# Kernel optimization log

Measured on AMD Instinct MI355X. Metric: run time of the kernel, lower is better.

The kernel has to match this reference:

```python
import jax, jax.numpy as jnp
import numpy as np

EPS = 1e-5
SINKHORN_ITERS = 20
ALPHA_INIT = 0.01


def setup_inputs() -> dict:
    key = jax.random.key(0)
    ks = jax.random.split(key, 8)
    B, n, C = 8192, 4, 2048
    nC = n * C
    return {
        "x_expanded": jax.random.normal(ks[0], (B, n, C), dtype=jnp.float32),
        "rmsnorm_weight": jnp.ones((C,), dtype=jnp.float32),
        "phi_pre": 0.02 * jax.random.normal(ks[1], (n, nC), dtype=jnp.float32),
        "phi_post": 0.02 * jax.random.normal(ks[2], (n, nC), dtype=jnp.float32),
        "phi_res": 0.02 * jax.random.normal(ks[3], (n * n, nC), dtype=jnp.float32),
        "b_pre": jnp.zeros((n,), dtype=jnp.float32),
        "b_post": jnp.zeros((n,), dtype=jnp.float32),
        "b_res": jnp.zeros((n, n), dtype=jnp.float32),
        "alpha_pre": jnp.float32(ALPHA_INIT),
        "alpha_post": jnp.float32(ALPHA_INIT),
        "alpha_res": jnp.float32(ALPHA_INIT),
    }


def _rmsnorm(x, w, eps):
    # RMSNorm over the channel dim C of each stream
    ms = jnp.mean(x * x, axis=-1, keepdims=True)
    return x * jax.lax.rsqrt(ms + eps) * w


def _sinkhorn(logits, iters, eps):
    # logits: (B, n, n) -> doubly-stochastic matrix via Sinkhorn-Knopp
    m = jnp.exp(logits - jnp.max(logits, axis=(1, 2), keepdims=True))
    for _ in range(iters):
        m = m / (jnp.sum(m, axis=2, keepdims=True) + eps)  # row normalize
        m = m / (jnp.sum(m, axis=1, keepdims=True) + eps)  # col normalize
    return m


def reference(x_expanded, rmsnorm_weight, phi_pre, phi_post, phi_res,
              b_pre, b_post, b_res, alpha_pre, alpha_post, alpha_res):
    B, n, C = x_expanded.shape
    x_norm = _rmsnorm(x_expanded, rmsnorm_weight, EPS)   # (B, n, C)
    xf = x_norm.reshape(B, n * C)                         # (B, nC)

    # dynamic mixing coefficients from learned projections
    h_pre = alpha_pre * (xf @ phi_pre.T) + b_pre          # (B, n)
    h_post = alpha_post * (xf @ phi_post.T) + b_post      # (B, n)
    h_res_logits = (alpha_res * (xf @ phi_res.T) + b_res.reshape(-1)).reshape(B, n, n)

    h_res = _sinkhorn(h_res_logits, SINKHORN_ITERS, EPS)  # (B, n, n) doubly stochastic

    # blended mixing of the raw residual streams
    mixed = jnp.einsum('bij,bjc->bic', h_res, x_expanded)        # (B, n, C)
    agg = jnp.einsum('bn,bnc->bc', h_pre, x_expanded)            # (B, C)
    out = mixed + h_post[:, :, None] * agg[:, None, :]           # (B, n, C)
    return out
```

## Files before the change

### kernel.cpp

```cpp
#include <hip/hip_runtime.h>
#include <hip/hip_bf16.h>
#include <cstdint>

#define CH 2048
#define NCF 8192
#define NJ 24
#define RPB 4
#define EPS_F 1e-5f
#define SINK_ITERS 20

typedef float v4f __attribute__((ext_vector_type(4)));

__device__ __forceinline__ uint32_t bf16rne(float f) {
    uint32_t u = __float_as_uint(f);
    return (u + 0x7fffu + ((u >> 16) & 1u)) >> 16;
}

__device__ __forceinline__ float dot8(const uint4& x, const uint4& p, float acc) {
    asm("v_dot2_f32_bf16 %0, %1, %2, %0" : "+v"(acc) : "v"(x.x), "v"(p.x));
    asm("v_dot2_f32_bf16 %0, %1, %2, %0" : "+v"(acc) : "v"(x.y), "v"(p.y));
    asm("v_dot2_f32_bf16 %0, %1, %2, %0" : "+v"(acc) : "v"(x.z), "v"(p.z));
    asm("v_dot2_f32_bf16 %0, %1, %2, %0" : "+v"(acc) : "v"(x.w), "v"(p.w));
    return acc;
}

__global__ void __launch_bounds__(256) prep_phi_kernel(
    const float* __restrict__ w,
    const float* __restrict__ phi_pre,
    const float* __restrict__ phi_post,
    const float* __restrict__ phi_res,
    const float* __restrict__ alpha_pre,
    const float* __restrict__ alpha_post,
    const float* __restrict__ alpha_res,
    uint16_t* __restrict__ phiW)
{
    int idx = blockIdx.x * 256 + threadIdx.x;
    if (idx >= NJ * NCF) return;
    int j = idx / NCF;
    int k = idx - j * NCF;
    int c = k & (CH - 1);
    float v, a;
    if (j < 4)      { v = phi_pre[j * NCF + k];        a = alpha_pre[0]; }
    else if (j < 8) { v = phi_post[(j - 4) * NCF + k]; a = alpha_post[0]; }
    else            { v = phi_res[(j - 8) * NCF + k];  a = alpha_res[0]; }
    phiW[idx] = (uint16_t)bf16rne(v * a * w[c]);
}

__global__ void __launch_bounds__(512) mhc_main_kernel(
    const float* __restrict__ x,
    const uint16_t* __restrict__ phiW,
    const float* __restrict__ b_pre,
    const float* __restrict__ b_post,
    const float* __restrict__ b_res,
    float* __restrict__ out)
{
    const int t = threadIdx.x;
    const int lane = t & 63;
    const int wave = t >> 6;
    const long b0 = (long)blockIdx.x * RPB;

    __shared__ uint32_t xn[RPB][NCF / 2];
    __shared__ float4 red[RPB][8];
    __shared__ float H[RPB][24];
    __shared__ float MS[RPB][16];

    {
        const float4* xp = reinterpret_cast<const float4*>(x + b0 * NCF);
        #pragma unroll
        for (int r = 0; r < RPB; ++r) {
            float ss0, ss1, ss2, ss3;
            {
                float4 a0 = xp[r * 2048 + t];
                float4 a1 = xp[r * 2048 + t + 512];
                float4 a2 = xp[r * 2048 + t + 1024];
                float4 a3 = xp[r * 2048 + t + 1536];
                ss0 = a0.x*a0.x + a0.y*a0.y + a0.z*a0.z + a0.w*a0.w;
                ss1 = a1.x*a1.x + a1.y*a1.y + a1.z*a1.z + a1.w*a1.w;
                ss2 = a2.x*a2.x + a2.y*a2.y + a2.z*a2.z + a2.w*a2.w;
                ss3 = a3.x*a3.x + a3.y*a3.y + a3.z*a3.z + a3.w*a3.w;
                *reinterpret_cast<uint2*>(&xn[r][2*t]) =
                    make_uint2(bf16rne(a0.x) | (bf16rne(a0.y) << 16),
                               bf16rne(a0.z) | (bf16rne(a0.w) << 16));
                *reinterpret_cast<uint2*>(&xn[r][2*t + 1024]) =
                    make_uint2(bf16rne(a1.x) | (bf16rne(a1.y) << 16),
                               bf16rne(a1.z) | (bf16rne(a1.w) << 16));
                *reinterpret_cast<uint2*>(&xn[r][2*t + 2048]) =
                    make_uint2(bf16rne(a2.x) | (bf16rne(a2.y) << 16),
                               bf16rne(a2.z) | (bf16rne(a2.w) << 16));
                *reinterpret_cast<uint2*>(&xn[r][2*t + 3072]) =
                    make_uint2(bf16rne(a3.x) | (bf16rne(a3.y) << 16),
                               bf16rne(a3.z) | (bf16rne(a3.w) << 16));
            }
            #pragma unroll
            for (int m = 1; m < 64; m <<= 1) {
                ss0 += __shfl_xor(ss0, m, 64);
                ss1 += __shfl_xor(ss1, m, 64);
                ss2 += __shfl_xor(ss2, m, 64);
                ss3 += __shfl_xor(ss3, m, 64);
            }
            if (lane == 0) red[r][wave] = make_float4(ss0, ss1, ss2, ss3);
        }
    }
    __syncthreads();

    float scl[RPB][4];
    #pragma unroll
    for (int r = 0; r < RPB; ++r) {
        float sx = 0.f, sy = 0.f, sz = 0.f, sw = 0.f;
        #pragma unroll
        for (int w8 = 0; w8 < 8; ++w8) {
            float4 v = red[r][w8];
            sx += v.x; sy += v.y; sz += v.z; sw += v.w;
        }
        scl[r][0] = rsqrtf(sx * (1.0f / CH) + EPS_F);
        scl[r][1] = rsqrtf(sy * (1.0f / CH) + EPS_F);
        scl[r][2] = rsqrtf(sz * (1.0f / CH) + EPS_F);
        scl[r][3] = rsqrtf(sw * (1.0f / CH) + EPS_F);
    }

    float accT[3][RPB] = {};
    float accS[3][RPB] = {};
    {
        const uint16_t* pw = phiW + (size_t)(wave * 3) * NCF;
        const int kl = 8 * lane;
        const uint4* xr0 = reinterpret_cast<const uint4*>(xn[0]);
        const uint4* xr1 = reinterpret_cast<const uint4*>(xn[1]);
        const uint4* xr2 = reinterpret_cast<const uint4*>(xn[2]);
        const uint4* xr3 = reinterpret_cast<const uint4*>(xn[3]);

        uint4 pbuf[3][3];
        uint4 xbuf[2][4];

        #pragma unroll
        for (int jl = 0; jl < 3; ++jl) {
            pbuf[0][jl] = *reinterpret_cast<const uint4*>(pw + jl * NCF + kl);
            pbuf[1][jl] = *reinterpret_cast<const uint4*>(pw + jl * NCF + 512 + kl);
        }
        xbuf[0][0] = xr0[lane]; xbuf[0][1] = xr1[lane];
        xbuf[0][2] = xr2[lane]; xbuf[0][3] = xr3[lane];

        #pragma unroll
        for (int u = 0; u < 16; ++u) {
            const int cur = u % 3;
            const int nxt = (u + 2) % 3;
            const int xc = u & 1;
            const int xq = (u + 1) & 1;
            if (u + 1 < 16) {
                const int i1 = 64 * (u + 1) + lane;
                xbuf[xq][0] = xr0[i1]; xbuf[xq][1] = xr1[i1];
                xbuf[xq][2] = xr2[i1]; xbuf[xq][3] = xr3[i1];
            }
            if (u + 2 < 16) {
                const int k2 = 512 * (u + 2) + kl;
                #pragma unroll
                for (int jl = 0; jl < 3; ++jl)
                    pbuf[nxt][jl] = *reinterpret_cast<const uint4*>(pw + jl * NCF + k2);
            }
            #pragma unroll
            for (int jl = 0; jl < 3; ++jl) {
                accS[jl][0] = dot8(xbuf[xc][0], pbuf[cur][jl], accS[jl][0]);
                accS[jl][1] = dot8(xbuf[xc][1], pbuf[cur][jl], accS[jl][1]);
                accS[jl][2] = dot8(xbuf[xc][2], pbuf[cur][jl], accS[jl][2]);
                accS[jl][3] = dot8(xbuf[xc][3], pbuf[cur][jl], accS[jl][3]);
            }
            if ((u & 3) == 3) {
                const int s = u >> 2;
                #pragma unroll
                for (int jl = 0; jl < 3; ++jl) {
                    #pragma unroll
                    for (int r = 0; r < RPB; ++r) {
                        accT[jl][r] = fmaf(scl[r][s], accS[jl][r], accT[jl][r]);
                        accS[jl][r] = 0.f;
                    }
                }
            }
        }
    }
    {
        #pragma unroll
        for (int m = 1; m < 64; m <<= 1) {
            #pragma unroll
            for (int jl = 0; jl < 3; ++jl) {
                #pragma unroll
                for (int r = 0; r < RPB; ++r)
                    accT[jl][r] += __shfl_xor(accT[jl][r], m, 64);
            }
        }
        if (lane == 0) {
            #pragma unroll
            for (int jl = 0; jl < 3; ++jl) {
                int j = 3 * wave + jl;
                float bias;
                if (j < 4)      bias = b_pre[j];
                else if (j < 8) bias = b_post[j - 4];
                else            bias = b_res[j - 8];
                #pragma unroll
                for (int r = 0; r < RPB; ++r) H[r][j] = accT[jl][r] + bias;
            }
        }
    }
    __syncthreads();

    {
        const int r = lane >> 4;
        const int q = lane & 15;
        float L = H[r][8 + q];
        float mx = L;
        mx = fmaxf(mx, __shfl_xor(mx, 1, 64));
        mx = fmaxf(mx, __shfl_xor(mx, 2, 64));
        mx = fmaxf(mx, __shfl_xor(mx, 4, 64));
        mx = fmaxf(mx, __shfl_xor(mx, 8, 64));
        float m = __expf(L - mx);
        #pragma unroll
        for (int it = 0; it < SINK_ITERS; ++it) {
            float rs = m + __shfl_xor(m, 1, 64);
            rs += __shfl_xor(rs, 2, 64);
            m = m * __builtin_amdgcn_rcpf(rs + EPS_F);
            float cs = m + __shfl_xor(m, 4, 64);
            cs += __shfl_xor(cs, 8, 64);
            m = m * __builtin_amdgcn_rcpf(cs + EPS_F);
        }
        MS[r][q] = m;
    }

    #pragma unroll
    for (int r = 0; r < RPB; ++r) {
        const float4 hp = *reinterpret_cast<const float4*>(&H[r][0]);
        const float4 hq = *reinterpret_cast<const float4*>(&H[r][4]);
        float4 hrm[4];
        #pragma unroll
        for (int i = 0; i < 4; ++i)
            hrm[i] = *reinterpret_cast<const float4*>(&MS[r][4 * i]);
        float4 s[4];
        #pragma unroll
        for (int jj = 0; jj < 4; ++jj) {
            uint2 pk = *reinterpret_cast<const uint2*>(&xn[r][2 * t + 1024 * jj]);
            s[jj].x = __uint_as_float(pk.x << 16);
            s[jj].y = __uint_as_float(pk.x & 0xffff0000u);
            s[jj].z = __uint_as_float(pk.y << 16);
            s[jj].w = __uint_as_float(pk.y & 0xffff0000u);
        }
        float ax = hp.x*s[0].x + hp.y*s[1].x + hp.z*s[2].x + hp.w*s[3].x;
        float ay = hp.x*s[0].y + hp.y*s[1].y + hp.z*s[2].y + hp.w*s[3].y;
        float az = hp.x*s[0].z + hp.y*s[1].z + hp.z*s[2].z + hp.w*s[3].z;
        float aw = hp.x*s[0].w + hp.y*s[1].w + hp.z*s[2].w + hp.w*s[3].w;
        const float hqv[4] = {hq.x, hq.y, hq.z, hq.w};
        v4f* op = reinterpret_cast<v4f*>(out + (b0 + r) * NCF + 4 * t);
        #pragma unroll
        for (int i = 0; i < 4; ++i) {
            v4f o;
            o.x = hrm[i].x*s[0].x + hrm[i].y*s[1].x + hrm[i].z*s[2].x + hrm[i].w*s[3].x + hqv[i]*ax;
            o.y = hrm[i].x*s[0].y + hrm[i].y*s[1].y + hrm[i].z*s[2].y + hrm[i].w*s[3].y + hqv[i]*ay;
            o.z = hrm[i].x*s[0].z + hrm[i].y*s[1].z + hrm[i].z*s[2].z + hrm[i].w*s[3].z + hqv[i]*az;
            o.w = hrm[i].x*s[0].w + hrm[i].y*s[1].w + hrm[i].z*s[2].w + hrm[i].w*s[3].w + hqv[i]*aw;
            __builtin_nontemporal_store(o, op + i * 512);
        }
    }
}

extern "C" void kernel_launch(void* const* d_in, const int* in_sizes, int n_in,
                              void* d_out, int out_size, void* d_ws, size_t ws_size,
                              hipStream_t stream)
{
    const float* x        = (const float*)d_in[0];
    const float* w        = (const float*)d_in[1];
    const float* phi_pre  = (const float*)d_in[2];
    const float* phi_post = (const float*)d_in[3];
    const float* phi_res  = (const float*)d_in[4];
    const float* b_pre    = (const float*)d_in[5];
    const float* b_post   = (const float*)d_in[6];
    const float* b_res    = (const float*)d_in[7];
    const float* a_pre    = (const float*)d_in[8];
    const float* a_post   = (const float*)d_in[9];
    const float* a_res    = (const float*)d_in[10];
    float* out = (float*)d_out;
    uint16_t* phiW = (uint16_t*)d_ws;

    const int B = in_sizes[0] / NCF;

    prep_phi_kernel<<<(NJ * NCF + 255) / 256, 256, 0, stream>>>(
        w, phi_pre, phi_post, phi_res, a_pre, a_post, a_res, phiW);

    mhc_main_kernel<<<B / RPB, 512, 0, stream>>>(
        x, phiW, b_pre, b_post, b_res, out);
}
```

Measured before the change: 157.5 us.

## Quantize activations and projection weights to int8 and use int8 dot products

Replaces the bf16 staging of x and the folded phi weights with per-row and per-stream absmax int8 quantization. The projection GEMV now uses v_dot4_i32_i8 with integer accumulators. The output mixing reads the int8 values and folds the dequant scales into a fused mixing matrix. The change halves the LDS footprint and the packed-weight traffic, but adds an extra absmax pre-pass kernel and a second global read of x. It also noticeably lowers accuracy on the output path, which risks failing tolerance.

```diff
diff --git a/kernel.cpp b/kernel.cpp
--- a/kernel.cpp
+++ b/kernel.cpp
@@ -11,20 +11,17 @@
 
 typedef float v4f __attribute__((ext_vector_type(4)));
 
-__device__ __forceinline__ uint32_t bf16rne(float f) {
-    uint32_t u = __float_as_uint(f);
-    return (u + 0x7fffu + ((u >> 16) & 1u)) >> 16;
-}
-
-__device__ __forceinline__ float dot8(const uint4& x, const uint4& p, float acc) {
-    asm("v_dot2_f32_bf16 %0, %1, %2, %0" : "+v"(acc) : "v"(x.x), "v"(p.x));
-    asm("v_dot2_f32_bf16 %0, %1, %2, %0" : "+v"(acc) : "v"(x.y), "v"(p.y));
-    asm("v_dot2_f32_bf16 %0, %1, %2, %0" : "+v"(acc) : "v"(x.z), "v"(p.z));
-    asm("v_dot2_f32_bf16 %0, %1, %2, %0" : "+v"(acc) : "v"(x.w), "v"(p.w));
-    return acc;
-}
-
-__global__ void __launch_bounds__(256) prep_phi_kernel(
+__device__ __forceinline__ int dot4i8(uint32_t a, uint32_t b, int c) {
+#if __has_builtin(__builtin_amdgcn_sdot4)
+    return __builtin_amdgcn_sdot4((int)a, (int)b, c, false);
+#else
+    int d;
+    asm("v_dot4_i32_i8 %0, %1, %2, %3" : "=v"(d) : "v"(a), "v"(b), "v"(c));
+    return d;
+#endif
+}
+
+__global__ void __launch_bounds__(256) prep_amax_kernel(
     const float* __restrict__ w,
     const float* __restrict__ phi_pre,
     const float* __restrict__ phi_post,
@@ -32,7 +29,36 @@
     const float* __restrict__ alpha_pre,
     const float* __restrict__ alpha_post,
     const float* __restrict__ alpha_res,
-    uint16_t* __restrict__ phiW)
+    float* __restrict__ amaxphi)
+{
+    const int j = blockIdx.x;
+    const int t = threadIdx.x;
+    const float* src; float a;
+    if (j < 4)      { src = phi_pre  + (size_t)j * NCF;       a = alpha_pre[0]; }
+    else if (j < 8) { src = phi_post + (size_t)(j-4) * NCF;   a = alpha_post[0]; }
+    else            { src = phi_res  + (size_t)(j-8) * NCF;   a = alpha_res[0]; }
+    float m = 0.f;
+    for (int k = t; k < NCF; k += 256)
+        m = fmaxf(m, fabsf(src[k] * a * w[k & (CH - 1)]));
+    #pragma unroll
+    for (int s = 1; s < 64; s <<= 1) m = fmaxf(m, __shfl_xor(m, s, 64));
+    __shared__ float wm[4];
+    if ((t & 63) == 0) wm[t >> 6] = m;
+    __syncthreads();
+    if (t == 0)
+        amaxphi[j] = fmaxf(fmaxf(fmaxf(wm[0], wm[1]), fmaxf(wm[2], wm[3])), 1e-30f);
+}
+
+__global__ void __launch_bounds__(256) prep_quant_kernel(
+    const float* __restrict__ w,
+    const float* __restrict__ phi_pre,
+    const float* __restrict__ phi_post,
+    const float* __restrict__ phi_res,
+    const float* __restrict__ alpha_pre,
+    const float* __restrict__ alpha_post,
+    const float* __restrict__ alpha_res,
+    const float* __restrict__ amaxphi,
+    int8_t* __restrict__ qphi)
 {
     int idx = blockIdx.x * 256 + threadIdx.x;
     if (idx >= NJ * NCF) return;
@@ -43,12 +69,15 @@
     if (j < 4)      { v = phi_pre[j * NCF + k];        a = alpha_pre[0]; }
     else if (j < 8) { v = phi_post[(j - 4) * NCF + k]; a = alpha_post[0]; }
     else            { v = phi_res[(j - 8) * NCF + k];  a = alpha_res[0]; }
-    phiW[idx] = (uint16_t)bf16rne(v * a * w[c]);
+    float f = v * a * w[c] * (127.0f / amaxphi[j]);
+    f = fminf(fmaxf(f, -127.0f), 127.0f);
+    qphi[idx] = (int8_t)(int)__builtin_rintf(f);
 }
 
 __global__ void __launch_bounds__(512) mhc_main_kernel(
     const float* __restrict__ x,
-    const uint16_t* __restrict__ phiW,
+    const int8_t* __restrict__ qphi,
+    const float* __restrict__ amaxphi,
     const float* __restrict__ b_pre,
     const float* __restrict__ b_post,
     const float* __restrict__ b_res,
@@ -59,132 +88,144 @@
     const int wave = t >> 6;
     const long b0 = (long)blockIdx.x * RPB;
 
-    __shared__ uint32_t xn[RPB][NCF / 2];
-    __shared__ float4 red[RPB][8];
-    __shared__ float H[RPB][24];
-    __shared__ float MS[RPB][16];
-
-    {
-        const float4* xp = reinterpret_cast<const float4*>(x + b0 * NCF);
-        #pragma unroll
-        for (int r = 0; r < RPB; ++r) {
-            float ss0, ss1, ss2, ss3;
-            {
-                float4 a0 = xp[r * 2048 + t];
-                float4 a1 = xp[r * 2048 + t + 512];
-                float4 a2 = xp[r * 2048 + t + 1024];
-                float4 a3 = xp[r * 2048 + t + 1536];
-                ss0 = a0.x*a0.x + a0.y*a0.y + a0.z*a0.z + a0.w*a0.w;
-                ss1 = a1.x*a1.x + a1.y*a1.y + a1.z*a1.z + a1.w*a1.w;
-                ss2 = a2.x*a2.x + a2.y*a2.y + a2.z*a2.z + a2.w*a2.w;
-                ss3 = a3.x*a3.x + a3.y*a3.y + a3.z*a3.z + a3.w*a3.w;
-                *reinterpret_cast<uint2*>(&xn[r][2*t]) =
-                    make_uint2(bf16rne(a0.x) | (bf16rne(a0.y) << 16),
-                               bf16rne(a0.z) | (bf16rne(a0.w) << 16));
-                *reinterpret_cast<uint2*>(&xn[r][2*t + 1024]) =
-                    make_uint2(bf16rne(a1.x) | (bf16rne(a1.y) << 16),
-                               bf16rne(a1.z) | (bf16rne(a1.w) << 16));
-                *reinterpret_cast<uint2*>(&xn[r][2*t + 2048]) =
-                    make_uint2(bf16rne(a2.x) | (bf16rne(a2.y) << 16),
-                               bf16rne(a2.z) | (bf16rne(a2.w) << 16));
-                *reinterpret_cast<uint2*>(&xn[r][2*t + 3072]) =
-                    make_uint2(bf16rne(a3.x) | (bf16rne(a3.y) << 16),
-                               bf16rne(a3.z) | (bf16rne(a3.w) << 16));
-            }
-            #pragma unroll
-            for (int m = 1; m < 64; m <<= 1) {
-                ss0 += __shfl_xor(ss0, m, 64);
-                ss1 += __shfl_xor(ss1, m, 64);
-                ss2 += __shfl_xor(ss2, m, 64);
-                ss3 += __shfl_xor(ss3, m, 64);
-            }
-            if (lane == 0) red[r][wave] = make_float4(ss0, ss1, ss2, ss3);
-        }
-    }
-    __syncthreads();
-
-    float scl[RPB][4];
+    __shared__ uint32_t xn8[RPB][NCF / 4];
+    __shared__ float4 redSS[RPB][8];
+    __shared__ float4 redAM[RPB][8];
+    __shared__ float H[RPB][24] __attribute__((aligned(16)));
+    __shared__ float MS[RPB][16] __attribute__((aligned(16)));
+
+    const float4* xp = reinterpret_cast<const float4*>(x + b0 * NCF);
+
     #pragma unroll
     for (int r = 0; r < RPB; ++r) {
-        float sx = 0.f, sy = 0.f, sz = 0.f, sw = 0.f;
-        #pragma unroll
-        for (int w8 = 0; w8 < 8; ++w8) {
-            float4 v = red[r][w8];
-            sx += v.x; sy += v.y; sz += v.z; sw += v.w;
-        }
-        scl[r][0] = rsqrtf(sx * (1.0f / CH) + EPS_F);
-        scl[r][1] = rsqrtf(sy * (1.0f / CH) + EPS_F);
-        scl[r][2] = rsqrtf(sz * (1.0f / CH) + EPS_F);
-        scl[r][3] = rsqrtf(sw * (1.0f / CH) + EPS_F);
-    }
+        float4 a0 = xp[r * 2048 + t];
+        float4 a1 = xp[r * 2048 + t + 512];
+        float4 a2 = xp[r * 2048 + t + 1024];
+        float4 a3 = xp[r * 2048 + t + 1536];
+        float ss0 = a0.x*a0.x + a0.y*a0.y + a0.z*a0.z + a0.w*a0.w;
+        float ss1 = a1.x*a1.x + a1.y*a1.y + a1.z*a1.z + a1.w*a1.w;
+        float ss2 = a2.x*a2.x + a2.y*a2.y + a2.z*a2.z + a2.w*a2.w;
+        float ss3 = a3.x*a3.x + a3.y*a3.y + a3.z*a3.z + a3.w*a3.w;
+        float m0 = fmaxf(fmaxf(fabsf(a0.x), fabsf(a0.y)), fmaxf(fabsf(a0.z), fabsf(a0.w)));
+        float m1 = fmaxf(fmaxf(fabsf(a1.x), fabsf(a1.y)), fmaxf(fabsf(a1.z), fabsf(a1.w)));
+        float m2 = fmaxf(fmaxf(fabsf(a2.x), fabsf(a2.y)), fmaxf(fabsf(a2.z), fabsf(a2.w)));
+        float m3 = fmaxf(fmaxf(fabsf(a3.x), fabsf(a3.y)), fmaxf(fabsf(a3.z), fabsf(a3.w)));
+        #pragma unroll
+        for (int s = 1; s < 64; s <<= 1) {
+            ss0 += __shfl_xor(ss0, s, 64); ss1 += __shfl_xor(ss1, s, 64);
+            ss2 += __shfl_xor(ss2, s, 64); ss3 += __shfl_xor(ss3, s, 64);
+            m0 = fmaxf(m0, __shfl_xor(m0, s, 64));
+            m1 = fmaxf(m1, __shfl_xor(m1, s, 64));
+            m2 = fmaxf(m2, __shfl_xor(m2, s, 64));
+            m3 = fmaxf(m3, __shfl_xor(m3, s, 64));
+        }
+        if (lane == 0) {
+            redSS[r][wave] = make_float4(ss0, ss1, ss2, ss3);
+            redAM[r][wave] = make_float4(m0, m1, m2, m3);
+        }
+    }
+    __syncthreads();
+
+    #pragma unroll
+    for (int r = 0; r < RPB; ++r) {
+        float qs[4];
+        #pragma unroll
+        for (int s = 0; s < 4; ++s) {
+            float am = 1e-30f;
+            #pragma unroll
+            for (int w8 = 0; w8 < 8; ++w8)
+                am = fmaxf(am, ((const float*)&redAM[r][w8])[s]);
+            qs[s] = 127.0f / am;
+        }
+        #pragma unroll
+        for (int jj = 0; jj < 4; ++jj) {
+            float4 v = xp[r * 2048 + t + 512 * jj];
+            const float q = qs[jj];
+            int q0 = (int)__builtin_rintf(fminf(fmaxf(v.x * q, -127.f), 127.f));
+            int q1 = (int)__builtin_rintf(fminf(fmaxf(v.y * q, -127.f), 127.f));
+            int q2 = (int)__builtin_rintf(fminf(fmaxf(v.z * q, -127.f), 127.f));
+            int q3 = (int)__builtin_rintf(fminf(fmaxf(v.w * q, -127.f), 127.f));
+            xn8[r][t + 512 * jj] = (uint32_t)(q0 & 255) | ((uint32_t)(q1 & 255) << 8)
+                                 | ((uint32_t)(q2 & 255) << 16) | ((uint32_t)(q3 & 255) << 24);
+        }
+    }
+    __syncthreads();
 
     float accT[3][RPB] = {};
-    float accS[3][RPB] = {};
+    int   accS[3][RPB] = {};
     {
-        const uint16_t* pw = phiW + (size_t)(wave * 3) * NCF;
+        const int8_t* pw = qphi + (size_t)(wave * 3) * NCF;
+        float aphi[3];
+        #pragma unroll
+        for (int jl = 0; jl < 3; ++jl)
+            aphi[jl] = amaxphi[3 * wave + jl] * (1.0f / 127.0f);
         const int kl = 8 * lane;
-        const uint4* xr0 = reinterpret_cast<const uint4*>(xn[0]);
-        const uint4* xr1 = reinterpret_cast<const uint4*>(xn[1]);
-        const uint4* xr2 = reinterpret_cast<const uint4*>(xn[2]);
-        const uint4* xr3 = reinterpret_cast<const uint4*>(xn[3]);
-
-        uint4 pbuf[3][3];
-        uint4 xbuf[2][4];
-
-        #pragma unroll
-        for (int jl = 0; jl < 3; ++jl) {
-            pbuf[0][jl] = *reinterpret_cast<const uint4*>(pw + jl * NCF + kl);
-            pbuf[1][jl] = *reinterpret_cast<const uint4*>(pw + jl * NCF + 512 + kl);
-        }
-        xbuf[0][0] = xr0[lane]; xbuf[0][1] = xr1[lane];
-        xbuf[0][2] = xr2[lane]; xbuf[0][3] = xr3[lane];
+        const uint2* xw0 = reinterpret_cast<const uint2*>(xn8[0]);
+        const uint2* xw1 = reinterpret_cast<const uint2*>(xn8[1]);
+        const uint2* xw2 = reinterpret_cast<const uint2*>(xn8[2]);
+        const uint2* xw3 = reinterpret_cast<const uint2*>(xn8[3]);
+
+        uint2 pA0 = *reinterpret_cast<const uint2*>(pw + 0 * NCF + kl);
+        uint2 pA1 = *reinterpret_cast<const uint2*>(pw + 1 * NCF + kl);
+        uint2 pA2 = *reinterpret_cast<const uint2*>(pw + 2 * NCF + kl);
 
         #pragma unroll
         for (int u = 0; u < 16; ++u) {
-            const int cur = u % 3;
-            const int nxt = (u + 2) % 3;
-            const int xc = u & 1;
-            const int xq = (u + 1) & 1;
+            uint2 pN0, pN1, pN2;
             if (u + 1 < 16) {
-                const int i1 = 64 * (u + 1) + lane;
-                xbuf[xq][0] = xr0[i1]; xbuf[xq][1] = xr1[i1];
-                xbuf[xq][2] = xr2[i1]; xbuf[xq][3] = xr3[i1];
+                const int kN = 512 * (u + 1) + kl;
+                pN0 = *reinterpret_cast<const uint2*>(pw + 0 * NCF + kN);
+                pN1 = *reinterpret_cast<const uint2*>(pw + 1 * NCF + kN);
+                pN2 = *reinterpret_cast<const uint2*>(pw + 2 * NCF + kN);
             }
-            if (u + 2 < 16) {
-                const int k2 = 512 * (u + 2) + kl;
+            const int xi = 64 * u + lane;
+            uint2 x0 = xw0[xi], x1 = xw1[xi], x2 = xw2[xi], x3 = xw3[xi];
+
+            accS[0][0] = dot4i8(x0.y, pA0.y, dot4i8(x0.x, pA0.x, accS[0][0]));
+            accS[0][1] = dot4i8(x1.y, pA0.y, dot4i8(x1.x, pA0.x, accS[0][1]));
+            accS[0][2] = dot4i8(x2.y, pA0.y, dot4i8(x2.x, pA0.x, accS[0][2]));
+            accS[0][3] = dot4i8(x3.y, pA0.y, dot4i8(x3.x, pA0.x, accS[0][3]));
+            accS[1][0] = dot4i8(x0.y, pA1.y, dot4i8(x0.x, pA1.x, accS[1][0]));
+            accS[1][1] = dot4i8(x1.y, pA1.y, dot4i8(x1.x, pA1.x, accS[1][1]));
+            accS[1][2] = dot4i8(x2.y, pA1.y, dot4i8(x2.x, pA1.x, accS[1][2]));
+            accS[1][3] = dot4i8(x3.y, pA1.y, dot4i8(x3.x, pA1.x, accS[1][3]));
+            accS[2][0] = dot4i8(x0.y, pA2.y, dot4i8(x0.x, pA2.x, accS[2][0]));
+            accS[2][1] = dot4i8(x1.y, pA2.y, dot4i8(x1.x, pA2.x, accS[2][1]));
+            accS[2][2] = dot4i8(x2.y, pA2.y, dot4i8(x2.x, pA2.x, accS[2][2]));
+            accS[2][3] = dot4i8(x3.y, pA2.y, dot4i8(x3.x, pA2.x, accS[2][3]));
+
+            if ((u & 3) == 3) {
+                const int s = u >> 2;
+                float cx[RPB];
+                #pragma unroll
+                for (int r = 0; r < RPB; ++r) {
+                    float ss = 0.f, am = 1e-30f;
+                    #pragma unroll
+                    for (int w8 = 0; w8 < 8; ++w8) {
+                        ss += ((const float*)&redSS[r][w8])[s];
+                        am = fmaxf(am, ((const float*)&redAM[r][w8])[s]);
+                    }
+                    cx[r] = rsqrtf(ss * (1.0f / CH) + EPS_F) * (am * (1.0f / 127.0f));
+                }
                 #pragma unroll
                 for (int jl = 0; jl < 3; ++jl)
-                    pbuf[nxt][jl] = *reinterpret_cast<const uint4*>(pw + jl * NCF + k2);
-            }
-            #pragma unroll
-            for (int jl = 0; jl < 3; ++jl) {
-                accS[jl][0] = dot8(xbuf[xc][0], pbuf[cur][jl], accS[jl][0]);
-                accS[jl][1] = dot8(xbuf[xc][1], pbuf[cur][jl], accS[jl][1]);
-                accS[jl][2] = dot8(xbuf[xc][2], pbuf[cur][jl], accS[jl][2]);
-                accS[jl][3] = dot8(xbuf[xc][3], pbuf[cur][jl], accS[jl][3]);
-            }
-            if ((u & 3) == 3) {
-                const int s = u >> 2;
-                #pragma unroll
-                for (int jl = 0; jl < 3; ++jl) {
                     #pragma unroll
                     for (int r = 0; r < RPB; ++r) {
-                        accT[jl][r] = fmaf(scl[r][s], accS[jl][r], accT[jl][r]);
-                        accS[jl][r] = 0.f;
+                        accT[jl][r] = fmaf(cx[r] * aphi[jl], (float)accS[jl][r], accT[jl][r]);
+                        accS[jl][r] = 0;
                     }
-                }
             }
+            pA0 = pN0; pA1 = pN1; pA2 = pN2;
         }
     }
     {
         #pragma unroll
-        for (int m = 1; m < 64; m <<= 1) {
+        for (int s = 1; s < 64; s <<= 1) {
             #pragma unroll
-            for (int jl = 0; jl < 3; ++jl) {
+            for (int jl = 0; jl < 3; ++jl)
                 #pragma unroll
                 for (int r = 0; r < RPB; ++r)
-                    accT[jl][r] += __shfl_xor(accT[jl][r], m, 64);
-            }
+                    accT[jl][r] += __shfl_xor(accT[jl][r], s, 64);
         }
         if (lane == 0) {
             #pragma unroll
@@ -227,32 +268,42 @@
     for (int r = 0; r < RPB; ++r) {
         const float4 hp = *reinterpret_cast<const float4*>(&H[r][0]);
         const float4 hq = *reinterpret_cast<const float4*>(&H[r][4]);
-        float4 hrm[4];
-        #pragma unroll
-        for (int i = 0; i < 4; ++i)
-            hrm[i] = *reinterpret_cast<const float4*>(&MS[r][4 * i]);
+        float dq[4];
+        #pragma unroll
+        for (int s = 0; s < 4; ++s) {
+            float am = 1e-30f;
+            #pragma unroll
+            for (int w8 = 0; w8 < 8; ++w8)
+                am = fmaxf(am, ((const float*)&redAM[r][w8])[s]);
+            dq[s] = am * (1.0f / 127.0f);
+        }
+        float4 M[4];
+        #pragma unroll
+        for (int i = 0; i < 4; ++i) {
+            float4 hrm = *reinterpret_cast<const float4*>(&MS[r][4 * i]);
+            const float qv = (i == 0) ? hq.x : (i == 1) ? hq.y : (i == 2) ? hq.z : hq.w;
+            M[i].x = fmaf(qv, hp.x, hrm.x) * dq[0];
+            M[i].y = fmaf(qv, hp.y, hrm.y) * dq[1];
+            M[i].z = fmaf(qv, hp.z, hrm.z) * dq[2];
+            M[i].w = fmaf(qv, hp.w, hrm.w) * dq[3];
+        }
         float4 s[4];
         #pragma unroll
         for (int jj = 0; jj < 4; ++jj) {
-            uint2 pk = *reinterpret_cast<const uint2*>(&xn[r][2 * t + 1024 * jj]);
-            s[jj].x = __uint_as_float(pk.x << 16);
-            s[jj].y = __uint_as_float(pk.x & 0xffff0000u);
-            s[jj].z = __uint_as_float(pk.y << 16);
-            s[jj].w = __uint_as_float(pk.y & 0xffff0000u);
-        }
-        float ax = hp.x*s[0].x + hp.y*s[1].x + hp.z*s[2].x + hp.w*s[3].x;
-        float ay = hp.x*s[0].y + hp.y*s[1].y + hp.z*s[2].y + hp.w*s[3].y;
-        float az = hp.x*s[0].z + hp.y*s[1].z + hp.z*s[2].z + hp.w*s[3].z;
-        float aw = hp.x*s[0].w + hp.y*s[1].w + hp.z*s[2].w + hp.w*s[3].w;
-        const float hqv[4] = {hq.x, hq.y, hq.z, hq.w};
+            uint32_t pk = xn8[r][t + 512 * jj];
+            s[jj].x = (float)((int)(pk << 24) >> 24);
+            s[jj].y = (float)((int)(pk << 16) >> 24);
+            s[jj].z = (float)((int)(pk << 8) >> 24);
+            s[jj].w = (float)((int)pk >> 24);
+        }
         v4f* op = reinterpret_cast<v4f*>(out + (b0 + r) * NCF + 4 * t);
         #pragma unroll
         for (int i = 0; i < 4; ++i) {
             v4f o;
-            o.x = hrm[i].x*s[0].x + hrm[i].y*s[1].x + hrm[i].z*s[2].x + hrm[i].w*s[3].x + hqv[i]*ax;
-            o.y = hrm[i].x*s[0].y + hrm[i].y*s[1].y + hrm[i].z*s[2].y + hrm[i].w*s[3].y + hqv[i]*ay;
-            o.z = hrm[i].x*s[0].z + hrm[i].y*s[1].z + hrm[i].z*s[2].z + hrm[i].w*s[3].z + hqv[i]*az;
-            o.w = hrm[i].x*s[0].w + hrm[i].y*s[1].w + hrm[i].z*s[2].w + hrm[i].w*s[3].w + hqv[i]*aw;
+            o.x = M[i].x*s[0].x + M[i].y*s[1].x + M[i].z*s[2].x + M[i].w*s[3].x;
+            o.y = M[i].x*s[0].y + M[i].y*s[1].y + M[i].z*s[2].y + M[i].w*s[3].y;
+            o.z = M[i].x*s[0].z + M[i].y*s[1].z + M[i].z*s[2].z + M[i].w*s[3].z;
+            o.w = M[i].x*s[0].w + M[i].y*s[1].w + M[i].z*s[2].w + M[i].w*s[3].w;
             __builtin_nontemporal_store(o, op + i * 512);
         }
     }
@@ -274,13 +325,18 @@
     const float* a_post   = (const float*)d_in[9];
     const float* a_res    = (const float*)d_in[10];
     float* out = (float*)d_out;
-    uint16_t* phiW = (uint16_t*)d_ws;
+
+    int8_t* qphi   = (int8_t*)d_ws;
+    float* amaxphi = (float*)((char*)d_ws + (size_t)NJ * NCF);
 
     const int B = in_sizes[0] / NCF;
 
-    prep_phi_kernel<<<(NJ * NCF + 255) / 256, 256, 0, stream>>>(
-        w, phi_pre, phi_post, phi_res, a_pre, a_post, a_res, phiW);
+    prep_amax_kernel<<<NJ, 256, 0, stream>>>(
+        w, phi_pre, phi_post, phi_res, a_pre, a_post, a_res, amaxphi);
+
+    prep_quant_kernel<<<(NJ * NCF + 255) / 256, 256, 0, stream>>>(
+        w, phi_pre, phi_post, phi_res, a_pre, a_post, a_res, amaxphi, qphi);
 
     mhc_main_kernel<<<B / RPB, 512, 0, stream>>>(
-        x, phiW, b_pre, b_post, b_res, out);
-}
+        x, qphi, amaxphi, b_pre, b_post, b_res, out);
+}
```

Result: slower. 197.6 us (+25.5%).
